# Optimization experiments

Hardware: AMD Instinct MI355X
Metric: run time of the kernel (lower is better)

The kernel has to match this reference:

```python
import jax, jax.numpy as jnp
import numpy as np

LN_EPS = 1e-12


def setup_inputs() -> dict:
    key = jax.random.key(0)
    ks = jax.random.split(key, 5)
    B, N, D_IN, D_OUT, E = 32, 2048, 128, 128, 64
    return {
        "x": jax.random.normal(ks[0], (B, N, D_IN), dtype=jnp.float32),
        "node_embeddings": jax.random.normal(ks[1], (N, E), dtype=jnp.float32),
        "time_embeddings": jax.random.normal(ks[2], (E,), dtype=jnp.float32),
        "weights_pool": jax.random.normal(ks[3], (E, 2, D_IN, D_OUT), dtype=jnp.float32) * 0.02,
        "bias_pool": jax.random.normal(ks[4], (E, D_OUT), dtype=jnp.float32) * 0.02,
        "ln_weight": jnp.ones((E,), dtype=jnp.float32),
        "ln_bias": jnp.zeros((E,), dtype=jnp.float32),
    }


def reference(x, node_embeddings, time_embeddings, weights_pool, bias_pool, ln_weight, ln_bias):
    # e: [N, E] = LayerNorm(node_emb + time_emb)  (dropout in eval mode = identity)
    e = node_embeddings + time_embeddings[None, :]
    mu = jnp.mean(e, axis=-1, keepdims=True)
    var = jnp.mean(jnp.square(e - mu), axis=-1, keepdims=True)
    e = (e - mu) * jax.lax.rsqrt(var + LN_EPS) * ln_weight + ln_bias

    # adaptive adjacency: softmax over rows of e @ e.T  -> [N, N]
    adj = jax.nn.softmax(jnp.einsum('nd,md->nm', e, e), axis=1)

    # per-node weights [N, 2, I, O] and bias [N, O]
    weights = jnp.einsum('nd,dkio->nkio', e, weights_pool)
    bias = e @ bias_pool  # [N, O]

    # supports: k=0 identity (x itself), k=1 adjacency aggregation
    x_agg = jnp.einsum('nm,bmc->bnc', adj, x)        # [B, N, I]
    x_g = jnp.stack([x, x_agg], axis=2)              # [B, N, 2, I]

    # per-node batched GEMM + bias
    out = jnp.einsum('bnki,nkio->bno', x_g, weights) + bias
    return out
```

## Files before the change

### kernel.cpp

```cpp
#include <hip/hip_runtime.h>


typedef unsigned short u16;
typedef unsigned int u32;
typedef __attribute__((ext_vector_type(8))) short bf16x8;
typedef __attribute__((ext_vector_type(4))) float f32x4;

#define NN 2048
#define EE 64
#define CC 128
#define BB 32

__device__ __forceinline__ u16 f2bf(float f) {
  u32 u = __builtin_bit_cast(u32, f);
  u += 0x7fffu + ((u >> 16) & 1u);
  return (u16)(u >> 16);
}

__device__ __forceinline__ f32x4 mfma16(bf16x8 a, bf16x8 b, f32x4 c) {
  return __builtin_amdgcn_mfma_f32_16x16x32_bf16(a, b, c, 0, 0, 0);
}

__global__ __launch_bounds__(64) void k_prep(
    const float* __restrict__ ne, const float* __restrict__ te,
    const float* __restrict__ lnw, const float* __restrict__ lnb,
    const float* __restrict__ bias_pool,
    float* __restrict__ e, u16* __restrict__ e_bf, float* __restrict__ bias_out) {
  int n = blockIdx.x;
  int d = threadIdx.x;
  float v = ne[n * EE + d] + te[d];
  float s = v;
#pragma unroll
  for (int off = 32; off > 0; off >>= 1) s += __shfl_xor(s, off);
  float mean = s * (1.0f / 64.0f);
  float c = v - mean;
  float q = c * c;
#pragma unroll
  for (int off = 32; off > 0; off >>= 1) q += __shfl_xor(q, off);
  float inv = rsqrtf(q * (1.0f / 64.0f) + 1e-12f);
  float ev = c * inv * lnw[d] + lnb[d];
  e[n * EE + d] = ev;
  e_bf[n * EE + d] = f2bf(ev);
  __shared__ float sh[64];
  sh[d] = ev;
  __syncthreads();
#pragma unroll
  for (int oo = 0; oo < 2; ++oo) {
    int o = oo * 64 + d;
    float acc = 0.f;
#pragma unroll 8
    for (int dd = 0; dd < 64; ++dd) acc += sh[dd] * bias_pool[dd * CC + o];
    bias_out[n * CC + o] = acc;
  }
}

__global__ __launch_bounds__(256) void k_poolt(const float* __restrict__ pool,
                                               u16* __restrict__ pool_r) {
  __shared__ float t[128 * 65];
  int ki = blockIdx.x;
  int tid = threadIdx.x;
  for (int it = 0; it < 32; ++it) {
    int idx = it * 256 + tid;
    int d = idx >> 7, o = idx & 127;
    t[o * 65 + d] = pool[d * 32768 + ki * 128 + o];
  }
  __syncthreads();
  for (int it = 0; it < 32; ++it) {
    int idx = it * 256 + tid;
    int o = idx >> 6, d = idx & 63;
    pool_r[((size_t)o * 256 + ki) * 64 + d] = f2bf(t[o * 65 + d]);
  }
}

__global__ __launch_bounds__(256) void k_xtrans(const float* __restrict__ x,
                                                u16* __restrict__ x_t,
                                                u16* __restrict__ x_bf) {
  __shared__ u16 t[128 * 68];
  int b = blockIdx.x >> 5;
  int m0 = (blockIdx.x & 31) * 64;
  int tid = threadIdx.x;
  for (int it = 0; it < 32; ++it) {
    int idx = it * 256 + tid;
    int m = idx >> 7, c = idx & 127;
    float v = x[(b * NN + m0 + m) * CC + c];
    u16 h = f2bf(v);
    x_bf[(b * NN + m0 + m) * CC + c] = h;
    t[c * 68 + m] = h;
  }
  __syncthreads();
  for (int it = 0; it < 32; ++it) {
    int idx = it * 256 + tid;
    int c = idx >> 6, m = idx & 63;
    x_t[(b * CC + c) * NN + m0 + m] = t[c * 68 + m];
  }
}

__global__ __launch_bounds__(256) void k_S(const float* __restrict__ e,
                                           float* __restrict__ S) {
  extern __shared__ float sm[];
  float* er = sm;
  float* ec = sm + 128 * 68;
  int n0 = (blockIdx.x >> 4) * 128, m0 = (blockIdx.x & 15) * 128;
  int tid = threadIdx.x;
  for (int it = 0; it < 32; ++it) {
    int idx = it * 256 + tid;
    int r = idx >> 6, d = idx & 63;
    er[r * 68 + d] = e[(n0 + r) * EE + d];
    ec[r * 68 + d] = e[(m0 + r) * EE + d];
  }
  __syncthreads();
  int tx = tid & 15, ty = tid >> 4;
  float acc[8][8] = {};
  for (int d4 = 0; d4 < 64; d4 += 4) {
    f32x4 av[8], bv[8];
#pragma unroll
    for (int i = 0; i < 8; ++i) av[i] = *(const f32x4*)&er[(ty + 16 * i) * 68 + d4];
#pragma unroll
    for (int j = 0; j < 8; ++j) bv[j] = *(const f32x4*)&ec[(tx + 16 * j) * 68 + d4];
#pragma unroll
    for (int i = 0; i < 8; ++i)
#pragma unroll
      for (int j = 0; j < 8; ++j) {
        acc[i][j] += av[i][0] * bv[j][0];
        acc[i][j] += av[i][1] * bv[j][1];
        acc[i][j] += av[i][2] * bv[j][2];
        acc[i][j] += av[i][3] * bv[j][3];
      }
  }
#pragma unroll
  for (int i = 0; i < 8; ++i)
#pragma unroll
    for (int j = 0; j < 8; ++j)
      S[(n0 + ty + 16 * i) * NN + m0 + tx + 16 * j] = acc[i][j];
}

__global__ __launch_bounds__(256) void k_softmax(const float* __restrict__ S,
                                                 u16* __restrict__ adj) {
  int n = blockIdx.x;
  int tid = threadIdx.x;
  int lane = tid & 63, w = tid >> 6;
  __shared__ float red[8];
  const f32x4* Srow = (const f32x4*)(S + (size_t)n * NN);
  f32x4 v0 = Srow[tid];
  f32x4 v1 = Srow[256 + tid];
  float mx = v0[0];
#pragma unroll
  for (int k = 1; k < 4; ++k) mx = fmaxf(mx, v0[k]);
#pragma unroll
  for (int k = 0; k < 4; ++k) mx = fmaxf(mx, v1[k]);
#pragma unroll
  for (int off = 32; off > 0; off >>= 1) mx = fmaxf(mx, __shfl_xor(mx, off));
  if (lane == 0) red[w] = mx;
  __syncthreads();
  mx = fmaxf(fmaxf(red[0], red[1]), fmaxf(red[2], red[3]));
  float ex[8];
  float sum = 0.f;
#pragma unroll
  for (int k = 0; k < 4; ++k) { ex[k] = __expf(v0[k] - mx); sum += ex[k]; }
#pragma unroll
  for (int k = 0; k < 4; ++k) { ex[4 + k] = __expf(v1[k] - mx); sum += ex[4 + k]; }
#pragma unroll
  for (int off = 32; off > 0; off >>= 1) sum += __shfl_xor(sum, off);
  if (lane == 0) red[4 + w] = sum;
  __syncthreads();
  sum = red[4] + red[5] + red[6] + red[7];
  float rs = 1.0f / sum;
  u16* arow = adj + (size_t)n * NN;
  u32 p0 = (u32)f2bf(ex[0] * rs) | ((u32)f2bf(ex[1] * rs) << 16);
  u32 p1 = (u32)f2bf(ex[2] * rs) | ((u32)f2bf(ex[3] * rs) << 16);
  ((uint2*)arow)[tid] = make_uint2(p0, p1);
  p0 = (u32)f2bf(ex[4] * rs) | ((u32)f2bf(ex[5] * rs) << 16);
  p1 = (u32)f2bf(ex[6] * rs) | ((u32)f2bf(ex[7] * rs) << 16);
  ((uint2*)arow)[256 + tid] = make_uint2(p0, p1);
}

__global__ __launch_bounds__(256) void k_aggr(const u16* __restrict__ adj,
                                              const u16* __restrict__ x_t,
                                              u16* __restrict__ xagg) {
  __shared__ u16 As[128 * 72];
  __shared__ u16 Bs[128 * 72];
  int mb = blockIdx.x & 15, b = blockIdx.x >> 4;
  int n0 = mb * 128;
  int tid = threadIdx.x;
  int lane = tid & 63, w = tid >> 6;
  int wm = w >> 1, wn = w & 1;
  int lm = lane & 15, lq = lane >> 4;
  f32x4 acc[4][4] = {};
  const u16* a_src = adj + (size_t)n0 * NN;
  const u16* b_src = x_t + (size_t)b * CC * NN;
  for (int kc = 0; kc < NN; kc += 64) {
    __syncthreads();
#pragma unroll
    for (int ii = 0; ii < 4; ++ii) {
      int idx = ii * 256 + tid;
      int row = idx >> 3, ch = idx & 7;
      *(bf16x8*)&As[row * 72 + ch * 8] = *(const bf16x8*)&a_src[(size_t)row * NN + kc + ch * 8];
      *(bf16x8*)&Bs[row * 72 + ch * 8] = *(const bf16x8*)&b_src[(size_t)row * NN + kc + ch * 8];
    }
    __syncthreads();
#pragma unroll
    for (int kk = 0; kk < 64; kk += 32) {
      bf16x8 af[4], bq[4];
#pragma unroll
      for (int i = 0; i < 4; ++i)
        af[i] = *(const bf16x8*)&As[(wm * 64 + i * 16 + lm) * 72 + kk + lq * 8];
#pragma unroll
      for (int j = 0; j < 4; ++j)
        bq[j] = *(const bf16x8*)&Bs[(wn * 64 + j * 16 + lm) * 72 + kk + lq * 8];
#pragma unroll
      for (int i = 0; i < 4; ++i)
#pragma unroll
        for (int j = 0; j < 4; ++j)
          acc[i][j] = mfma16(af[i], bq[j], acc[i][j]);
    }
  }
#pragma unroll
  for (int i = 0; i < 4; ++i) {
    int nr = n0 + wm * 64 + i * 16 + lq * 4;
#pragma unroll
    for (int j = 0; j < 4; ++j) {
      int c = wn * 64 + j * 16 + lm;
#pragma unroll
      for (int r = 0; r < 4; ++r)
        xagg[((size_t)b * NN + nr + r) * CC + c] = f2bf(acc[i][j][r]);
    }
  }
}

#define WL_OS 36
#define WL_NS 1192
__global__ __launch_bounds__(512, 4) void k_out(const u16* __restrict__ e_bf,
                                                const u16* __restrict__ pool_r,
                                                const u16* __restrict__ x_bf,
                                                const u16* __restrict__ xagg,
                                                const float* __restrict__ bias,
                                                float* __restrict__ out) {
  __shared__ u16 Wl[16 * WL_NS];
  int ng = blockIdx.x & 127, og = blockIdx.x >> 7;
  int n0 = ng * 16, o0 = og * 32;
  int tid = threadIdx.x;
  int lane = tid & 63, w = tid >> 6;
  int lm = lane & 15, lq = lane >> 4;
  bf16x8 e0 = *(const bf16x8*)&e_bf[(n0 + lm) * EE + lq * 8];
  bf16x8 e1 = *(const bf16x8*)&e_bf[(n0 + lm) * EE + 32 + lq * 8];
  f32x4 acc[2][2][2] = {};
  for (int c = 0; c < 8; ++c) {
#pragma unroll
    for (int oi = 0; oi < 4; ++oi) {
      int o = w * 4 + oi;
#pragma unroll
      for (int kh = 0; kh < 2; ++kh) {
        const u16* ap = pool_r + ((size_t)(o0 + o) * 256 + c * 32 + kh * 16 + lm) * 64 + lq * 8;
        bf16x8 p0 = *(const bf16x8*)ap;
        bf16x8 p1 = *(const bf16x8*)(ap + 32);
        f32x4 g = {0.f, 0.f, 0.f, 0.f};
        g = mfma16(p0, e0, g);
        g = mfma16(p1, e1, g);
        ushort4 h;
        h.x = f2bf(g[0]); h.y = f2bf(g[1]); h.z = f2bf(g[2]); h.w = f2bf(g[3]);
        *(ushort4*)&Wl[lm * WL_NS + o * WL_OS + kh * 16 + lq * 4] = h;
      }
    }
    __syncthreads();
#pragma unroll
    for (int nn = 0; nn < 2; ++nn) {
      int ndl = w * 2 + nn;
      int n = n0 + ndl;
      const u16* xs = (c < 4) ? x_bf : xagg;
      int ck = (c < 4) ? c * 32 : c * 32 - 128;
      bf16x8 a0 = *(const bf16x8*)&xs[((size_t)lm * NN + n) * CC + ck + lq * 8];
      bf16x8 a1 = *(const bf16x8*)&xs[(((size_t)16 + lm) * NN + n) * CC + ck + lq * 8];
#pragma unroll
      for (int nt = 0; nt < 2; ++nt) {
        bf16x8 bv = *(const bf16x8*)&Wl[ndl * WL_NS + (nt * 16 + lm) * WL_OS + lq * 8];
        acc[nn][0][nt] = mfma16(a0, bv, acc[nn][0][nt]);
        acc[nn][1][nt] = mfma16(a1, bv, acc[nn][1][nt]);
      }
    }
    __syncthreads();
  }
#pragma unroll
  for (int nn = 0; nn < 2; ++nn) {
    int n = n0 + w * 2 + nn;
#pragma unroll
    for (int nt = 0; nt < 2; ++nt) {
      int oc = o0 + nt * 16 + lm;
      float bv = bias[n * CC + oc];
#pragma unroll
      for (int mt = 0; mt < 2; ++mt) {
#pragma unroll
        for (int r = 0; r < 4; ++r) {
          int b = mt * 16 + lq * 4 + r;
          out[((size_t)b * NN + n) * CC + oc] = acc[nn][mt][nt][r] + bv;
        }
      }
    }
  }
}

extern "C" void kernel_launch(void* const* d_in, const int* in_sizes, int n_in,
                              void* d_out, int out_size, void* d_ws, size_t ws_size,
                              hipStream_t stream) {
  const float* x        = (const float*)d_in[0];
  const float* node_emb = (const float*)d_in[1];
  const float* time_emb = (const float*)d_in[2];
  const float* pool     = (const float*)d_in[3];
  const float* bias_pl  = (const float*)d_in[4];
  const float* ln_w     = (const float*)d_in[5];
  const float* ln_b     = (const float*)d_in[6];
  float* out = (float*)d_out;

  char* p = (char*)d_ws;
  auto alloc = [&](size_t bytes) {
    char* r = p;
    p += (bytes + 255) & ~(size_t)255;
    return r;
  };
  float* e      = (float*)alloc((size_t)NN * EE * 4);
  u16*   e_bf   = (u16*)  alloc((size_t)NN * EE * 2);
  float* biasb  = (float*)alloc((size_t)NN * CC * 4);
  u16*   adj    = (u16*)  alloc((size_t)NN * NN * 2);
  u16*   x_t    = (u16*)  alloc((size_t)BB * CC * NN * 2);
  u16*   x_bf   = (u16*)  alloc((size_t)BB * NN * CC * 2);
  u16*   pool_r = (u16*)  alloc((size_t)128 * 256 * 64 * 2);
  char*  Sx     = alloc((size_t)NN * NN * 4);
  float* S      = (float*)Sx;
  u16*   xagg   = (u16*)Sx;

  if (ws_size < (size_t)(p - (char*)d_ws)) return;

  (void)hipFuncSetAttribute((const void*)k_S, hipFuncAttributeMaxDynamicSharedMemorySize,
                            2 * 128 * 68 * 4);

  k_prep<<<NN, 64, 0, stream>>>(node_emb, time_emb, ln_w, ln_b, bias_pl, e, e_bf, biasb);
  k_poolt<<<256, 256, 0, stream>>>(pool, pool_r);
  k_xtrans<<<BB * 32, 256, 0, stream>>>(x, x_t, x_bf);
  k_S<<<256, 256, 2 * 128 * 68 * 4, stream>>>(e, S);
  k_softmax<<<NN, 256, 0, stream>>>(S, adj);
  k_aggr<<<16 * BB, 256, 0, stream>>>(adj, x_t, xagg);
  k_out<<<512, 512, 0, stream>>>(e_bf, pool_r, x_bf, xagg, biasb, out);
}
```

Baseline: 253.8 us.

## Double-buffer per-node weight generation in k_out and retile to 32 nodes x 16 outputs

Restructures the output kernel so per-node weights are generated into a double-buffered LDS tile. The pool loads for the next chunk are issued before the barrier, and the next chunk's weights are generated after this chunk's MFMAs, which removes one barrier per iteration and overlaps global loads with compute. The block tile changes from 16 nodes x 32 outputs to 32 nodes x 16 outputs, so each pool fragment is reused across two node tiles, and the LDS layout is changed to match. Shared memory doubles and register pressure rises, which may hurt occupancy under the 4-blocks-per-CU launch bound.

```diff
diff --git a/kernel.cpp b/kernel.cpp
--- a/kernel.cpp
+++ b/kernel.cpp
@@ -4,6 +4,7 @@
 typedef unsigned short u16;
 typedef unsigned int u32;
 typedef __attribute__((ext_vector_type(8))) short bf16x8;
+typedef __attribute__((ext_vector_type(4))) short bf16x4;
 typedef __attribute__((ext_vector_type(4))) float f32x4;
 
 #define NN 2048
@@ -227,74 +228,101 @@
   }
 }
 
-#define WL_OS 36
-#define WL_NS 1192
+#define PS 1156
+#define NS2 36
+#define BS (16 * PS)
 __global__ __launch_bounds__(512, 4) void k_out(const u16* __restrict__ e_bf,
                                                 const u16* __restrict__ pool_r,
                                                 const u16* __restrict__ x_bf,
                                                 const u16* __restrict__ xagg,
                                                 const float* __restrict__ bias,
                                                 float* __restrict__ out) {
-  __shared__ u16 Wl[16 * WL_NS];
-  int ng = blockIdx.x & 127, og = blockIdx.x >> 7;
-  int n0 = ng * 16, o0 = og * 32;
+  __shared__ u16 Wl[2 * BS];
+  int og = blockIdx.x & 7, ng = blockIdx.x >> 3;
+  int n0 = ng * 32, o0 = og * 16;
   int tid = threadIdx.x;
   int lane = tid & 63, w = tid >> 6;
   int lm = lane & 15, lq = lane >> 4;
-  bf16x8 e0 = *(const bf16x8*)&e_bf[(n0 + lm) * EE + lq * 8];
-  bf16x8 e1 = *(const bf16x8*)&e_bf[(n0 + lm) * EE + 32 + lq * 8];
-  f32x4 acc[2][2][2] = {};
+
+  bf16x8 eF[2][2];
+#pragma unroll
+  for (int nt = 0; nt < 2; ++nt)
+#pragma unroll
+    for (int dh = 0; dh < 2; ++dh)
+      eF[nt][dh] = *(const bf16x8*)&e_bf[(n0 + nt * 16 + lm) * EE + dh * 32 + lq * 8];
+
+  bf16x8 pf[2][2][2];
+  auto load_pool = [&](int cc) {
+#pragma unroll
+    for (int oi = 0; oi < 2; ++oi)
+#pragma unroll
+      for (int kh = 0; kh < 2; ++kh)
+#pragma unroll
+        for (int dh = 0; dh < 2; ++dh)
+          pf[oi][kh][dh] = *(const bf16x8*)&pool_r[
+              ((size_t)(o0 + w * 2 + oi) * 256 + cc * 32 + kh * 16 + lm) * 64 + dh * 32 + lq * 8];
+  };
+  auto do_gen = [&](int cc) {
+    int buf = cc & 1;
+#pragma unroll
+    for (int oi = 0; oi < 2; ++oi) {
+      int o = w * 2 + oi;
+#pragma unroll
+      for (int kh = 0; kh < 2; ++kh)
+#pragma unroll
+        for (int nt = 0; nt < 2; ++nt) {
+          f32x4 g = {0.f, 0.f, 0.f, 0.f};
+          g = mfma16(pf[oi][kh][0], eF[nt][0], g);
+          g = mfma16(pf[oi][kh][1], eF[nt][1], g);
+          ushort4 h;
+          h.x = f2bf(g[0]); h.y = f2bf(g[1]); h.z = f2bf(g[2]); h.w = f2bf(g[3]);
+          *(ushort4*)&Wl[buf * BS + o * PS + (nt * 16 + lm) * NS2 + kh * 16 + lq * 4] = h;
+        }
+    }
+  };
+
+  load_pool(0);
+  do_gen(0);
+  f32x4 acc[4][2] = {};
+
   for (int c = 0; c < 8; ++c) {
-#pragma unroll
-    for (int oi = 0; oi < 4; ++oi) {
-      int o = w * 4 + oi;
-#pragma unroll
-      for (int kh = 0; kh < 2; ++kh) {
-        const u16* ap = pool_r + ((size_t)(o0 + o) * 256 + c * 32 + kh * 16 + lm) * 64 + lq * 8;
-        bf16x8 p0 = *(const bf16x8*)ap;
-        bf16x8 p1 = *(const bf16x8*)(ap + 32);
-        f32x4 g = {0.f, 0.f, 0.f, 0.f};
-        g = mfma16(p0, e0, g);
-        g = mfma16(p1, e1, g);
-        ushort4 h;
-        h.x = f2bf(g[0]); h.y = f2bf(g[1]); h.z = f2bf(g[2]); h.w = f2bf(g[3]);
-        *(ushort4*)&Wl[lm * WL_NS + o * WL_OS + kh * 16 + lq * 4] = h;
+    int buf = c & 1;
+    const u16* xs = (c < 4) ? x_bf : xagg;
+    int ck = (c & 3) * 32;
+    bf16x8 xa[4][2];
+#pragma unroll
+    for (int nn = 0; nn < 4; ++nn) {
+      int n = n0 + w * 4 + nn;
+      xa[nn][0] = *(const bf16x8*)&xs[((size_t)lm * NN + n) * CC + ck + lq * 8];
+      xa[nn][1] = *(const bf16x8*)&xs[(((size_t)16 + lm) * NN + n) * CC + ck + lq * 8];
+    }
+    if (c < 7) load_pool(c + 1);
+    __syncthreads();
+#pragma unroll
+    for (int nn = 0; nn < 4; ++nn) {
+      int nd = w * 4 + nn;
+      int base = buf * BS + lm * PS + nd * NS2 + lq * 8;
+      bf16x4 b0 = *(const bf16x4*)&Wl[base];
+      bf16x4 b1 = *(const bf16x4*)&Wl[base + 4];
+      bf16x8 bv = __builtin_shufflevector(b0, b1, 0, 1, 2, 3, 4, 5, 6, 7);
+      acc[nn][0] = mfma16(xa[nn][0], bv, acc[nn][0]);
+      acc[nn][1] = mfma16(xa[nn][1], bv, acc[nn][1]);
+    }
+    if (c < 7) do_gen(c + 1);
+  }
+
+#pragma unroll
+  for (int nn = 0; nn < 4; ++nn) {
+    int n = n0 + w * 4 + nn;
+    int oc = o0 + lm;
+    float bv = bias[n * CC + oc];
+#pragma unroll
+    for (int mt = 0; mt < 2; ++mt)
+#pragma unroll
+      for (int r = 0; r < 4; ++r) {
+        int b = mt * 16 + lq * 4 + r;
+        out[((size_t)b * NN + n) * CC + oc] = acc[nn][mt][r] + bv;
       }
-    }
-    __syncthreads();
-#pragma unroll
-    for (int nn = 0; nn < 2; ++nn) {
-      int ndl = w * 2 + nn;
-      int n = n0 + ndl;
-      const u16* xs = (c < 4) ? x_bf : xagg;
-      int ck = (c < 4) ? c * 32 : c * 32 - 128;
-      bf16x8 a0 = *(const bf16x8*)&xs[((size_t)lm * NN + n) * CC + ck + lq * 8];
-      bf16x8 a1 = *(const bf16x8*)&xs[(((size_t)16 + lm) * NN + n) * CC + ck + lq * 8];
-#pragma unroll
-      for (int nt = 0; nt < 2; ++nt) {
-        bf16x8 bv = *(const bf16x8*)&Wl[ndl * WL_NS + (nt * 16 + lm) * WL_OS + lq * 8];
-        acc[nn][0][nt] = mfma16(a0, bv, acc[nn][0][nt]);
-        acc[nn][1][nt] = mfma16(a1, bv, acc[nn][1][nt]);
-      }
-    }
-    __syncthreads();
-  }
-#pragma unroll
-  for (int nn = 0; nn < 2; ++nn) {
-    int n = n0 + w * 2 + nn;
-#pragma unroll
-    for (int nt = 0; nt < 2; ++nt) {
-      int oc = o0 + nt * 16 + lm;
-      float bv = bias[n * CC + oc];
-#pragma unroll
-      for (int mt = 0; mt < 2; ++mt) {
-#pragma unroll
-        for (int r = 0; r < 4; ++r) {
-          int b = mt * 16 + lq * 4 + r;
-          out[((size_t)b * NN + n) * CC + oc] = acc[nn][mt][nt][r] + bv;
-        }
-      }
-    }
   }
 }
 
```

Result: slower. 304.7 us (+20.1%).

## Interleave x and x_agg per node, use direct global-to-LDS loads, retile k_out

Applied to the files above, without the earlier changes.

Introduces a node-major combined buffer xg_t [N, B, 256] that holds bf16 x and the aggregated x side by side. k_out can then read contiguous per-node A fragments instead of strided rows across batches. k_aggr now uses global_load_lds (direct global-to-LDS) with unpadded LDS tiles and writes into the combined buffer. k_out is retiled to 256-thread blocks over 16 output columns, with each wave covering 4 nodes and a 64-wide K chunk. The trade-offs are possible LDS bank conflicts from removing the padding, more blocks that each regenerate per-node weights, and S no longer sharing memory with xagg.

```diff
diff --git a/kernel.cpp b/kernel.cpp
--- a/kernel.cpp
+++ b/kernel.cpp
@@ -5,6 +5,8 @@
 typedef unsigned int u32;
 typedef __attribute__((ext_vector_type(8))) short bf16x8;
 typedef __attribute__((ext_vector_type(4))) float f32x4;
+typedef const __attribute__((address_space(1))) u16* gas1;
+typedef __attribute__((address_space(3))) u16* las3;
 
 #define NN 2048
 #define EE 64
@@ -74,7 +76,7 @@
 
 __global__ __launch_bounds__(256) void k_xtrans(const float* __restrict__ x,
                                                 u16* __restrict__ x_t,
-                                                u16* __restrict__ x_bf) {
+                                                u16* __restrict__ xg_t) {
   __shared__ u16 t[128 * 68];
   int b = blockIdx.x >> 5;
   int m0 = (blockIdx.x & 31) * 64;
@@ -82,16 +84,21 @@
   for (int it = 0; it < 32; ++it) {
     int idx = it * 256 + tid;
     int m = idx >> 7, c = idx & 127;
-    float v = x[(b * NN + m0 + m) * CC + c];
-    u16 h = f2bf(v);
-    x_bf[(b * NN + m0 + m) * CC + c] = h;
-    t[c * 68 + m] = h;
+    float v = x[((size_t)b * NN + m0 + m) * CC + c];
+    t[c * 68 + m] = f2bf(v);
   }
   __syncthreads();
   for (int it = 0; it < 32; ++it) {
     int idx = it * 256 + tid;
     int c = idx >> 6, m = idx & 63;
-    x_t[(b * CC + c) * NN + m0 + m] = t[c * 68 + m];
+    x_t[((size_t)b * CC + c) * NN + m0 + m] = t[c * 68 + m];
+  }
+  for (int it = 0; it < 16; ++it) {
+    int idx = it * 256 + tid;
+    int m = idx >> 6, c2 = idx & 63;
+    float2 v = *(const float2*)&x[((size_t)b * NN + m0 + m) * CC + c2 * 2];
+    u32 pk = (u32)f2bf(v.x) | ((u32)f2bf(v.y) << 16);
+    *(u32*)&xg_t[(((size_t)(m0 + m)) * 32 + b) * 256 + c2 * 2] = pk;
   }
 }
 
@@ -131,7 +138,7 @@
   for (int i = 0; i < 8; ++i)
 #pragma unroll
     for (int j = 0; j < 8; ++j)
-      S[(n0 + ty + 16 * i) * NN + m0 + tx + 16 * j] = acc[i][j];
+      S[(size_t)(n0 + ty + 16 * i) * NN + m0 + tx + 16 * j] = acc[i][j];
 }
 
 __global__ __launch_bounds__(256) void k_softmax(const float* __restrict__ S,
@@ -174,11 +181,11 @@
   ((uint2*)arow)[256 + tid] = make_uint2(p0, p1);
 }
 
-__global__ __launch_bounds__(256) void k_aggr(const u16* __restrict__ adj,
-                                              const u16* __restrict__ x_t,
-                                              u16* __restrict__ xagg) {
-  __shared__ u16 As[128 * 72];
-  __shared__ u16 Bs[128 * 72];
+__global__ __launch_bounds__(256, 3) void k_aggr(const u16* __restrict__ adj,
+                                                 const u16* __restrict__ x_t,
+                                                 u16* __restrict__ xg_t) {
+  __shared__ u16 As[128 * 64];
+  __shared__ u16 Bs[128 * 64];
   int mb = blockIdx.x & 15, b = blockIdx.x >> 4;
   int n0 = mb * 128;
   int tid = threadIdx.x;
@@ -194,8 +201,10 @@
     for (int ii = 0; ii < 4; ++ii) {
       int idx = ii * 256 + tid;
       int row = idx >> 3, ch = idx & 7;
-      *(bf16x8*)&As[row * 72 + ch * 8] = *(const bf16x8*)&a_src[(size_t)row * NN + kc + ch * 8];
-      *(bf16x8*)&Bs[row * 72 + ch * 8] = *(const bf16x8*)&b_src[(size_t)row * NN + kc + ch * 8];
+      __builtin_amdgcn_global_load_lds((gas1)(a_src + (size_t)row * NN + kc + ch * 8),
+                                       (las3)(As + (size_t)(ii * 256 + w * 64) * 8), 16, 0, 0);
+      __builtin_amdgcn_global_load_lds((gas1)(b_src + (size_t)row * NN + kc + ch * 8),
+                                       (las3)(Bs + (size_t)(ii * 256 + w * 64) * 8), 16, 0, 0);
     }
     __syncthreads();
 #pragma unroll
@@ -203,10 +212,10 @@
       bf16x8 af[4], bq[4];
 #pragma unroll
       for (int i = 0; i < 4; ++i)
-        af[i] = *(const bf16x8*)&As[(wm * 64 + i * 16 + lm) * 72 + kk + lq * 8];
+        af[i] = *(const bf16x8*)&As[(wm * 64 + i * 16 + lm) * 64 + kk + lq * 8];
 #pragma unroll
       for (int j = 0; j < 4; ++j)
-        bq[j] = *(const bf16x8*)&Bs[(wn * 64 + j * 16 + lm) * 72 + kk + lq * 8];
+        bq[j] = *(const bf16x8*)&Bs[(wn * 64 + j * 16 + lm) * 64 + kk + lq * 8];
 #pragma unroll
       for (int i = 0; i < 4; ++i)
 #pragma unroll
@@ -222,79 +231,71 @@
       int c = wn * 64 + j * 16 + lm;
 #pragma unroll
       for (int r = 0; r < 4; ++r)
-        xagg[((size_t)b * NN + nr + r) * CC + c] = f2bf(acc[i][j][r]);
-    }
-  }
-}
-
-#define WL_OS 36
-#define WL_NS 1192
-__global__ __launch_bounds__(512, 4) void k_out(const u16* __restrict__ e_bf,
+        xg_t[((size_t)(nr + r) * 32 + b) * 256 + 128 + c] = f2bf(acc[i][j][r]);
+    }
+  }
+}
+
+__global__ __launch_bounds__(256, 4) void k_out(const u16* __restrict__ e_bf,
                                                 const u16* __restrict__ pool_r,
-                                                const u16* __restrict__ x_bf,
-                                                const u16* __restrict__ xagg,
+                                                const u16* __restrict__ xg_t,
                                                 const float* __restrict__ bias,
                                                 float* __restrict__ out) {
-  __shared__ u16 Wl[16 * WL_NS];
+  __shared__ u16 Wl[16 * 1040];
   int ng = blockIdx.x & 127, og = blockIdx.x >> 7;
-  int n0 = ng * 16, o0 = og * 32;
+  int n0 = ng * 16, o0 = og * 16;
   int tid = threadIdx.x;
   int lane = tid & 63, w = tid >> 6;
   int lm = lane & 15, lq = lane >> 4;
-  bf16x8 e0 = *(const bf16x8*)&e_bf[(n0 + lm) * EE + lq * 8];
-  bf16x8 e1 = *(const bf16x8*)&e_bf[(n0 + lm) * EE + 32 + lq * 8];
-  f32x4 acc[2][2][2] = {};
-  for (int c = 0; c < 8; ++c) {
-#pragma unroll
-    for (int oi = 0; oi < 4; ++oi) {
-      int o = w * 4 + oi;
-#pragma unroll
-      for (int kh = 0; kh < 2; ++kh) {
-        const u16* ap = pool_r + ((size_t)(o0 + o) * 256 + c * 32 + kh * 16 + lm) * 64 + lq * 8;
-        bf16x8 p0 = *(const bf16x8*)ap;
-        bf16x8 p1 = *(const bf16x8*)(ap + 32);
-        f32x4 g = {0.f, 0.f, 0.f, 0.f};
-        g = mfma16(p0, e0, g);
-        g = mfma16(p1, e1, g);
-        ushort4 h;
-        h.x = f2bf(g[0]); h.y = f2bf(g[1]); h.z = f2bf(g[2]); h.w = f2bf(g[3]);
-        *(ushort4*)&Wl[lm * WL_NS + o * WL_OS + kh * 16 + lq * 4] = h;
+
+  bf16x8 eF0 = *(const bf16x8*)&e_bf[(n0 + lm) * EE + lq * 8];
+  bf16x8 eF1 = *(const bf16x8*)&e_bf[(n0 + lm) * EE + 32 + lq * 8];
+  f32x4 acc[4][2] = {};
+
+  for (int c = 0; c < 4; ++c) {
+    int t = c * 4 + w;
+#pragma unroll 8
+    for (int o = 0; o < 16; ++o) {
+      const u16* ap = pool_r + ((size_t)(o0 + o) * 256 + t * 16 + lm) * 64 + lq * 8;
+      bf16x8 p0 = *(const bf16x8*)ap;
+      bf16x8 p1 = *(const bf16x8*)(ap + 32);
+      f32x4 g = {0.f, 0.f, 0.f, 0.f};
+      g = mfma16(p0, eF0, g);
+      g = mfma16(p1, eF1, g);
+      ushort4 h;
+      h.x = f2bf(g[0]); h.y = f2bf(g[1]); h.z = f2bf(g[2]); h.w = f2bf(g[3]);
+      *(ushort4*)&Wl[lm * 1040 + o * 64 + w * 16 + lq * 4] = h;
+    }
+    __syncthreads();
+#pragma unroll
+    for (int nn = 0; nn < 4; ++nn) {
+      int nd = w * 4 + nn;
+      int n = n0 + nd;
+#pragma unroll
+      for (int ks = 0; ks < 2; ++ks) {
+        int kloc = c * 64 + ks * 32 + lq * 8;
+        bf16x8 a0 = *(const bf16x8*)&xg_t[((size_t)n * 32 + lm) * 256 + kloc];
+        bf16x8 a1 = *(const bf16x8*)&xg_t[((size_t)n * 32 + 16 + lm) * 256 + kloc];
+        bf16x8 bv = *(const bf16x8*)&Wl[nd * 1040 + lm * 64 + ks * 32 + lq * 8];
+        acc[nn][0] = mfma16(a0, bv, acc[nn][0]);
+        acc[nn][1] = mfma16(a1, bv, acc[nn][1]);
       }
     }
     __syncthreads();
-#pragma unroll
-    for (int nn = 0; nn < 2; ++nn) {
-      int ndl = w * 2 + nn;
-      int n = n0 + ndl;
-      const u16* xs = (c < 4) ? x_bf : xagg;
-      int ck = (c < 4) ? c * 32 : c * 32 - 128;
-      bf16x8 a0 = *(const bf16x8*)&xs[((size_t)lm * NN + n) * CC + ck + lq * 8];
-      bf16x8 a1 = *(const bf16x8*)&xs[(((size_t)16 + lm) * NN + n) * CC + ck + lq * 8];
-#pragma unroll
-      for (int nt = 0; nt < 2; ++nt) {
-        bf16x8 bv = *(const bf16x8*)&Wl[ndl * WL_NS + (nt * 16 + lm) * WL_OS + lq * 8];
-        acc[nn][0][nt] = mfma16(a0, bv, acc[nn][0][nt]);
-        acc[nn][1][nt] = mfma16(a1, bv, acc[nn][1][nt]);
+  }
+
+#pragma unroll
+  for (int nn = 0; nn < 4; ++nn) {
+    int n = n0 + w * 4 + nn;
+    int oc = o0 + lm;
+    float bv = bias[n * CC + oc];
+#pragma unroll
+    for (int mt = 0; mt < 2; ++mt)
+#pragma unroll
+      for (int r = 0; r < 4; ++r) {
+        int b = mt * 16 + lq * 4 + r;
+        out[((size_t)b * NN + n) * CC + oc] = acc[nn][mt][r] + bv;
       }
-    }
-    __syncthreads();
-  }
-#pragma unroll
-  for (int nn = 0; nn < 2; ++nn) {
-    int n = n0 + w * 2 + nn;
-#pragma unroll
-    for (int nt = 0; nt < 2; ++nt) {
-      int oc = o0 + nt * 16 + lm;
-      float bv = bias[n * CC + oc];
-#pragma unroll
-      for (int mt = 0; mt < 2; ++mt) {
-#pragma unroll
-        for (int r = 0; r < 4; ++r) {
-          int b = mt * 16 + lq * 4 + r;
-          out[((size_t)b * NN + n) * CC + oc] = acc[nn][mt][nt][r] + bv;
-        }
-      }
-    }
   }
 }
 
@@ -321,11 +322,9 @@
   float* biasb  = (float*)alloc((size_t)NN * CC * 4);
   u16*   adj    = (u16*)  alloc((size_t)NN * NN * 2);
   u16*   x_t    = (u16*)  alloc((size_t)BB * CC * NN * 2);
-  u16*   x_bf   = (u16*)  alloc((size_t)BB * NN * CC * 2);
+  u16*   xg_t   = (u16*)  alloc((size_t)NN * BB * 256 * 2);
   u16*   pool_r = (u16*)  alloc((size_t)128 * 256 * 64 * 2);
-  char*  Sx     = alloc((size_t)NN * NN * 4);
-  float* S      = (float*)Sx;
-  u16*   xagg   = (u16*)Sx;
+  float* S      = (float*)alloc((size_t)NN * NN * 4);
 
   if (ws_size < (size_t)(p - (char*)d_ws)) return;
 
@@ -334,9 +333,9 @@
 
   k_prep<<<NN, 64, 0, stream>>>(node_emb, time_emb, ln_w, ln_b, bias_pl, e, e_bf, biasb);
   k_poolt<<<256, 256, 0, stream>>>(pool, pool_r);
-  k_xtrans<<<BB * 32, 256, 0, stream>>>(x, x_t, x_bf);
+  k_xtrans<<<BB * 32, 256, 0, stream>>>(x, x_t, xg_t);
   k_S<<<256, 256, 2 * 128 * 68 * 4, stream>>>(e, S);
   k_softmax<<<NN, 256, 0, stream>>>(S, adj);
-  k_aggr<<<16 * BB, 256, 0, stream>>>(adj, x_t, xagg);
-  k_out<<<512, 512, 0, stream>>>(e_bf, pool_r, x_bf, xagg, biasb, out);
-}
+  k_aggr<<<16 * BB, 256, 0, stream>>>(adj, x_t, xg_t);
+  k_out<<<8 * 128, 256, 0, stream>>>(e_bf, pool_r, xg_t, biasb, out);
+}
```

New measurement: 277.7 us. 9.4% more time.
